# Kernel tuning notes

Hardware: AMD Instinct MI355X
Metric: run time of the kernel (lower is better)

The kernel has to match this reference:

```python
import jax, jax.numpy as jnp
import numpy as np

B = 16384      # batch (number of jagged segments)
T = 819200     # total jagged values per feature
V = 200000     # vocab per table
D0, D1 = 64, 128


def setup_inputs() -> dict:
    key = jax.random.key(0)
    ks = jax.random.split(key, 7)
    table0 = jax.random.normal(ks[0], (V, D0), jnp.float32) * 0.01
    table1 = jax.random.normal(ks[1], (V, D1), jnp.float32) * 0.01
    idx0 = jax.random.randint(ks[2], (T,), 0, V, dtype=jnp.int64)
    idx1 = jax.random.randint(ks[3], (T,), 0, V, dtype=jnp.int64)
    off0 = jnp.sort(jax.random.randint(ks[4], (B + 1,), 0, T, dtype=jnp.int64))
    off0 = off0.at[0].set(0).at[-1].set(T)
    off1 = jnp.sort(jax.random.randint(ks[5], (B + 1,), 0, T, dtype=jnp.int64))
    off1 = off1.at[0].set(0).at[-1].set(T)
    weights0 = jax.random.uniform(ks[6], (T,), jnp.float32)
    return {"table0": table0, "table1": table1, "weights0": weights0,
            "idx0": idx0, "idx1": idx1, "off0": off0, "off1": off1}


def _jagged_pool(emb, offsets, mode, patch_value):
    # emb: [T, D]; offsets: [B+1] with offsets[0]=0, offsets[-1]=T
    n = emb.shape[0]
    # segment id of each value: i such that offsets[i] <= j < offsets[i+1]
    seg = jnp.searchsorted(offsets, jnp.arange(n), side="right") - 1
    sums = jax.ops.segment_sum(emb, seg, num_segments=B)  # [B, D]
    counts = (offsets[1:] - offsets[:-1]).astype(emb.dtype)[:, None]  # [B, 1]
    nonempty = counts > 0
    patch = jnp.asarray(patch_value, emb.dtype)
    if mode == "mean":
        return jnp.where(nonempty, sums / jnp.maximum(counts, 1), patch)
    return jnp.where(nonempty, sums, patch)


def reference(table0, table1, weights0, idx0, idx1, off0, off1):
    emb0 = table0[idx0] * weights0[:, None]      # gather + weight, [T, D0]
    out0 = _jagged_pool(emb0, off0, "sum", 0.0)  # [B, D0]
    emb1 = table1[idx1]                          # [T, D1]
    out1 = _jagged_pool(emb1, off1, "mean", 0.0) # [B, D1]
    return (out0, out1)
```

## Files before the change

### kernel.cpp

```cpp
#include <hip/hip_runtime.h>

#define BATCH 16384

__global__ __launch_bounds__(192)
void combine_jagged_kernel(const float* __restrict__ table0,
                           const float* __restrict__ table1,
                           const float* __restrict__ w0,
                           const int* __restrict__ idx0,
                           const int* __restrict__ idx1,
                           const int* __restrict__ off0,
                           const int* __restrict__ off1,
                           float* __restrict__ out) {
    const int b    = blockIdx.x;
    const int wave = threadIdx.x >> 6;
    const int lane = threadIdx.x & 63;

    if (wave == 0) {
        const int s = __builtin_amdgcn_readfirstlane(off0[b]);
        const int e = __builtin_amdgcn_readfirstlane(off0[b + 1]);
        const float* tab = table0 + lane;
        float acc = 0.0f;
        int j = s;
        for (; j + 8 <= e; j += 8) {
            float v[8];
            #pragma unroll
            for (int k = 0; k < 8; ++k) {
                const int r = idx0[j + k];
                v[k] = tab[(size_t)r * 64];
            }
            #pragma unroll
            for (int k = 0; k < 8; ++k) {
                acc = fmaf(v[k], w0[j + k], acc);
            }
        }
        for (; j < e; ++j) {
            const int r = idx0[j];
            acc = fmaf(tab[(size_t)r * 64], w0[j], acc);
        }
        out[(size_t)b * 64 + lane] = acc;
    } else {
        const int s = __builtin_amdgcn_readfirstlane(off1[b]);
        const int e = __builtin_amdgcn_readfirstlane(off1[b + 1]);
        const int colbase = (wave - 1) * 64;
        const float* tab = table1 + colbase + lane;
        float acc = 0.0f;
        int j = s;
        for (; j + 8 <= e; j += 8) {
            float v[8];
            #pragma unroll
            for (int k = 0; k < 8; ++k) {
                const int r = idx1[j + k];
                v[k] = tab[(size_t)r * 128];
            }
            #pragma unroll
            for (int k = 0; k < 8; ++k) {
                acc += v[k];
            }
        }
        for (; j < e; ++j) {
            const int r = idx1[j];
            acc += tab[(size_t)r * 128];
        }
        const int cnt = e - s;
        const float inv = (cnt > 0) ? 1.0f / (float)cnt : 0.0f;
        out[(size_t)BATCH * 64 + (size_t)b * 128 + colbase + lane] = acc * inv;
    }
}

extern "C" void kernel_launch(void* const* d_in, const int* in_sizes, int n_in,
                              void* d_out, int out_size, void* d_ws, size_t ws_size,
                              hipStream_t stream) {
    const float* table0 = (const float*)d_in[0];
    const float* table1 = (const float*)d_in[1];
    const float* w0     = (const float*)d_in[2];
    const int*   idx0   = (const int*)d_in[3];
    const int*   idx1   = (const int*)d_in[4];
    const int*   off0   = (const int*)d_in[5];
    const int*   off1   = (const int*)d_in[6];
    float* out = (float*)d_out;

    combine_jagged_kernel<<<BATCH, 192, 0, stream>>>(
        table0, table1, w0, idx0, idx1, off0, off1, out);
}
```

Baseline: 272.1 us.

## Use float2 gathers with row-splitting across half-waves and index prefetch

Each lane now loads two floats per row, so one wave covers a row with half the lanes. For table0, the two half-waves take alternating rows and are combined with a cross-lane shuffle. For table1, the two waves take alternating rows across all 128 columns and are combined through shared memory. Indices and weights for the next 16 rows are prefetched before the current batch is accumulated, and the tail is handled with masked, clamped loads. This targets fewer, wider memory transactions and more loads in flight, at the cost of a __syncthreads, extra registers, and some wasted loads on masked tails.

```diff
diff --git a/kernel.cpp b/kernel.cpp
--- a/kernel.cpp
+++ b/kernel.cpp
@@ -1,6 +1,8 @@
 #include <hip/hip_runtime.h>
 
 #define BATCH 16384
+
+typedef float f2 __attribute__((ext_vector_type(2)));
 
 __global__ __launch_bounds__(192)
 void combine_jagged_kernel(const float* __restrict__ table0,
@@ -14,56 +16,115 @@
     const int b    = blockIdx.x;
     const int wave = threadIdx.x >> 6;
     const int lane = threadIdx.x & 63;
+    const int half = lane >> 5;
+    const int hl   = lane & 31;
+
+    __shared__ f2 red[64];
+
+    f2 acc = {0.0f, 0.0f};
+    float inv = 0.0f;
 
     if (wave == 0) {
         const int s = __builtin_amdgcn_readfirstlane(off0[b]);
         const int e = __builtin_amdgcn_readfirstlane(off0[b + 1]);
-        const float* tab = table0 + lane;
-        float acc = 0.0f;
+        const float* tab = table0 + hl * 2;
         int j = s;
-        for (; j + 8 <= e; j += 8) {
-            float v[8];
+        const int nfull = (e - s) >> 4;
+        if (nfull > 0) {
+            int rr[16]; float ww[16];
+            #pragma unroll
+            for (int k = 0; k < 16; ++k) { rr[k] = idx0[j + k]; ww[k] = w0[j + k]; }
+            for (int it = 0; it < nfull; ++it) {
+                f2 v[8]; float wk[8];
+                #pragma unroll
+                for (int k = 0; k < 8; ++k) {
+                    const int r = half ? rr[2 * k + 1] : rr[2 * k];
+                    wk[k] = half ? ww[2 * k + 1] : ww[2 * k];
+                    v[k] = *(const f2*)(tab + (size_t)r * 64);
+                }
+                j += 16;
+                if (it + 1 < nfull) {
+                    #pragma unroll
+                    for (int k = 0; k < 16; ++k) { rr[k] = idx0[j + k]; ww[k] = w0[j + k]; }
+                }
+                #pragma unroll
+                for (int k = 0; k < 8; ++k) acc += v[k] * wk[k];
+            }
+        }
+        const int rem = e - j;
+        if (rem > 0) {
+            int rr[16]; float ww[16];
+            #pragma unroll
+            for (int k = 0; k < 16; ++k) {
+                const int jk = j + (k < rem ? k : rem - 1);
+                rr[k] = idx0[jk];
+                ww[k] = (k < rem) ? w0[jk] : 0.0f;
+            }
+            f2 v[8]; float wk[8];
             #pragma unroll
             for (int k = 0; k < 8; ++k) {
-                const int r = idx0[j + k];
-                v[k] = tab[(size_t)r * 64];
+                const int r = half ? rr[2 * k + 1] : rr[2 * k];
+                wk[k] = half ? ww[2 * k + 1] : ww[2 * k];
+                v[k] = *(const f2*)(tab + (size_t)r * 64);
             }
             #pragma unroll
-            for (int k = 0; k < 8; ++k) {
-                acc = fmaf(v[k], w0[j + k], acc);
-            }
+            for (int k = 0; k < 8; ++k) acc += v[k] * wk[k];
         }
-        for (; j < e; ++j) {
-            const int r = idx0[j];
-            acc = fmaf(tab[(size_t)r * 64], w0[j], acc);
-        }
-        out[(size_t)b * 64 + lane] = acc;
+        acc.x += __shfl_xor(acc.x, 32, 64);
+        acc.y += __shfl_xor(acc.y, 32, 64);
     } else {
         const int s = __builtin_amdgcn_readfirstlane(off1[b]);
         const int e = __builtin_amdgcn_readfirstlane(off1[b + 1]);
-        const int colbase = (wave - 1) * 64;
-        const float* tab = table1 + colbase + lane;
-        float acc = 0.0f;
+        const int par = wave - 1;
+        const float* tab = table1 + lane * 2;
         int j = s;
-        for (; j + 8 <= e; j += 8) {
-            float v[8];
+        const int nfull = (e - s) >> 4;
+        if (nfull > 0) {
+            int rr[8];
+            #pragma unroll
+            for (int k = 0; k < 8; ++k) rr[k] = idx1[j + 2 * k + par];
+            for (int it = 0; it < nfull; ++it) {
+                f2 v[8];
+                #pragma unroll
+                for (int k = 0; k < 8; ++k) v[k] = *(const f2*)(tab + (size_t)rr[k] * 128);
+                j += 16;
+                if (it + 1 < nfull) {
+                    #pragma unroll
+                    for (int k = 0; k < 8; ++k) rr[k] = idx1[j + 2 * k + par];
+                }
+                #pragma unroll
+                for (int k = 0; k < 8; ++k) acc += v[k];
+            }
+        }
+        const int rem = e - j;
+        if (rem > 0) {
+            int rr[8]; float mk[8];
             #pragma unroll
             for (int k = 0; k < 8; ++k) {
-                const int r = idx1[j + k];
-                v[k] = tab[(size_t)r * 128];
+                const int o = 2 * k + par;
+                const int jo = j + (o < rem ? o : rem - 1);
+                rr[k] = idx1[jo];
+                mk[k] = (o < rem) ? 1.0f : 0.0f;
             }
+            f2 v[8];
             #pragma unroll
-            for (int k = 0; k < 8; ++k) {
-                acc += v[k];
-            }
-        }
-        for (; j < e; ++j) {
-            const int r = idx1[j];
-            acc += tab[(size_t)r * 128];
+            for (int k = 0; k < 8; ++k) v[k] = *(const f2*)(tab + (size_t)rr[k] * 128);
+            #pragma unroll
+            for (int k = 0; k < 8; ++k) acc += v[k] * mk[k];
         }
         const int cnt = e - s;
-        const float inv = (cnt > 0) ? 1.0f / (float)cnt : 0.0f;
-        out[(size_t)BATCH * 64 + (size_t)b * 128 + colbase + lane] = acc * inv;
+        inv = (cnt > 0) ? 1.0f / (float)cnt : 0.0f;
+        if (wave == 2) red[lane] = acc;
+    }
+
+    __syncthreads();
+
+    if (wave == 0) {
+        if (half == 0) *(f2*)(out + (size_t)b * 64 + hl * 2) = acc;
+    } else if (wave == 1) {
+        acc += red[lane];
+        acc *= inv;
+        *(f2*)(out + (size_t)BATCH * 64 + (size_t)b * 128 + lane * 2) = acc;
     }
 }
 
```

Result: faster. 260.2 us (-4.4%).
